# Kernel optimization log

Measured on AMD Instinct MI355X. Metric: run time of the kernel, lower is better.

The kernel has to match this reference:

```python
import jax, jax.numpy as jnp
import numpy as np

N_NODES = 100000
N_EDGES = 1600000
IN_FEATS = 128
HID = 128      # 2 * n_hidden
OUT = 64       # n_hidden


def setup_inputs() -> dict:
    key = jax.random.key(0)
    ks = jax.random.split(key, 10)
    features = jax.random.normal(ks[0], (N_NODES, IN_FEATS), dtype=jnp.float32)
    src = jax.random.randint(ks[1], (N_EDGES,), 0, N_NODES)
    dst = jax.random.randint(ks[2], (N_EDGES,), 0, N_NODES)
    s0 = 1.0 / np.sqrt(IN_FEATS)
    s1 = 1.0 / np.sqrt(HID)
    W_self0 = jax.random.uniform(ks[3], (IN_FEATS, HID), minval=-s0, maxval=s0, dtype=jnp.float32)
    W_neigh0 = jax.random.uniform(ks[4], (IN_FEATS, HID), minval=-s0, maxval=s0, dtype=jnp.float32)
    b0 = jnp.zeros((HID,), dtype=jnp.float32)
    W_self1 = jax.random.uniform(ks[5], (HID, OUT), minval=-s1, maxval=s1, dtype=jnp.float32)
    W_neigh1 = jax.random.uniform(ks[6], (HID, OUT), minval=-s1, maxval=s1, dtype=jnp.float32)
    b1 = jnp.zeros((OUT,), dtype=jnp.float32)
    return {"features": features, "src": src, "dst": dst,
            "W_self0": W_self0, "W_neigh0": W_neigh0, "b0": b0,
            "W_self1": W_self1, "W_neigh1": W_neigh1, "b1": b1}


def _mean_agg(x, src, dst, n_nodes):
    # gather neighbor feats along edges, sum per destination, divide by in-degree
    summed = jax.ops.segment_sum(x[src], dst, num_segments=n_nodes)  # [N, d]
    deg = jax.ops.segment_sum(jnp.ones((src.shape[0],), x.dtype), dst, num_segments=n_nodes)
    deg = jnp.maximum(deg, 1.0)[:, None]
    return summed / deg


def _sage_layer(x, src, dst, W_self, W_neigh, b, act):
    agg = _mean_agg(x, src, dst, x.shape[0])
    out = x @ W_self + agg @ W_neigh + b
    return jax.nn.relu(out) if act else out


def reference(features, src, dst, W_self0, W_neigh0, b0, W_self1, W_neigh1, b1):
    h = _sage_layer(features, src, dst, W_self0, W_neigh0, b0, act=True)
    h = _sage_layer(h, src, dst, W_self1, W_neigh1, b1, act=False)
    return h
```

## Files before the change

### kernel.cpp

```cpp
#include <hip/hip_runtime.h>

#define N_NODES 100000
#define N_EDGES 1600000
#define CAP 60
#define OVF_CAP 8192
#define GBLK 782
#define NBIN 1563
#define BINCAP2 1280
#define FBLK 12500
#define ZROW 100000

typedef unsigned int uint;
typedef unsigned short ushort;
typedef __attribute__((ext_vector_type(8))) short short8;
typedef __attribute__((ext_vector_type(4))) float f32x4;

__device__ __forceinline__ ushort f2bf(float f) {
  uint x = __float_as_uint(f);
  x += 0x7fffu + ((x >> 16) & 1u);
  return (ushort)(x >> 16);
}
__device__ __forceinline__ float bflo(uint u) {
  return __uint_as_float(u << 16);
}
__device__ __forceinline__ float bfhi(uint u) {
  return __uint_as_float(u & 0xffff0000u);
}
__device__ __forceinline__ f32x4 uplo(uint4 u) {
  return (f32x4){bflo(u.x), bfhi(u.x), bflo(u.y), bfhi(u.y)};
}
__device__ __forceinline__ f32x4 uphi(uint4 u) {
  return (f32x4){bflo(u.z), bfhi(u.z), bflo(u.w), bfhi(u.w)};
}

__global__ __launch_bounds__(256) void k_pb(
    const int* __restrict__ src, const int* __restrict__ dst,
    const float* __restrict__ feat, const float* __restrict__ Ws0,
    const float* __restrict__ Wn0, const float* __restrict__ Ws1,
    const float* __restrict__ Wn1, uint* __restrict__ gcursor,
    uint* __restrict__ binbuf, int* __restrict__ ovf_cnt,
    int* __restrict__ ovf, uint* __restrict__ fbfu, uint* __restrict__ hwu,
    ushort* __restrict__ wp0, ushort* __restrict__ wp1) {
  __shared__ uint hist[NBIN];
  int b = blockIdx.x;
  int tid = threadIdx.x;
  if (b < GBLK) {
    for (int i = tid; i < NBIN; i += 256) hist[i] = 0;
    __syncthreads();
    int e0 = b * 2048;
    uint val[8], bn[8], rk[8];
    int vld[8];
#pragma unroll
    for (int it = 0; it < 8; ++it) {
      int e = e0 + it * 256 + tid;
      vld[it] = (e < N_EDGES);
      if (vld[it]) {
        uint s = (uint)src[e];
        uint d = (uint)dst[e];
        bn[it] = d >> 6;
        rk[it] = atomicAdd(&hist[bn[it]], 1u);
        val[it] = s | ((d & 63u) << 17);
      }
    }
    __syncthreads();
    for (int i = tid; i < NBIN; i += 256) {
      uint h = hist[i];
      hist[i] = h ? atomicAdd(&gcursor[i * 16], h) : 0u;
    }
    __syncthreads();
#pragma unroll
    for (int it = 0; it < 8; ++it) {
      if (!vld[it]) continue;
      uint p = hist[bn[it]] + rk[it];
      if (p < BINCAP2) {
        binbuf[(size_t)bn[it] * BINCAP2 + p] = val[it];
      } else {
        int o = atomicAdd(ovf_cnt, 1);
        if (o < OVF_CAP) {
          ovf[2 * o] = (int)(val[it] & 0x1FFFFu);
          ovf[2 * o + 1] = (int)(bn[it] * 64 + (val[it] >> 17));
        }
      }
    }
    return;
  }
  if (b < GBLK + FBLK) {
    int i = (b - GBLK) * 256 + tid;
    float4 v = reinterpret_cast<const float4*>(feat)[i];
    uint2 o;
    o.x = (uint)f2bf(v.x) | ((uint)f2bf(v.y) << 16);
    o.y = (uint)f2bf(v.z) | ((uint)f2bf(v.w) << 16);
    reinterpret_cast<uint2*>(fbfu)[i] = o;
    return;
  }
  int wb = b - GBLK - FBLK;
  if (wb >= 192) {
    if (tid < 64) fbfu[ZROW * 64 + tid] = 0;
    else if (tid < 96) hwu[ZROW * 32 + (tid - 64)] = 0;
    return;
  }
  int idx = wb * 256 + tid;
  if (idx < 32768) {
    int k = idx >> 7, n = idx & 127;
    float v = (k < 128) ? Ws0[k * 128 + n] : Wn0[(k - 128) * 128 + n];
    int s = k >> 5, q = (k >> 3) & 3, j = k & 7;
    int t = n >> 4, c = n & 15;
    wp0[(((s * 8 + t) * 64) + (q * 16 + c)) * 8 + j] = f2bf(v);
  } else {
    int i2 = idx - 32768;
    int k = i2 >> 7, n = i2 & 127;
    float v = (n < 64) ? Wn1[k * 64 + n] : Ws1[k * 64 + (n - 64)];
    int s = k >> 5, q = (k >> 3) & 3, j = k & 7;
    int t = n >> 4, c = n & 15;
    wp1[(((s * 8 + t) * 64) + (q * 16 + c)) * 8 + j] = f2bf(v);
  }
}

__global__ __launch_bounds__(256) void k_agg0(
    const uint4* __restrict__ fbf4, const uint* __restrict__ binbuf,
    const uint* __restrict__ gcursor, int* __restrict__ ovf_cnt,
    int* __restrict__ ovf, uint4* __restrict__ agg4) {
  __shared__ __attribute__((aligned(16))) int lbkt[64 * CAP];
  __shared__ uint lcnt[64];
  int bb = blockIdx.x;
  int tid = threadIdx.x;
  if (tid < 64) lcnt[tid] = 0;
#pragma unroll
  for (int i = tid; i < 64 * CAP; i += 256) lbkt[i] = ZROW;
  __syncthreads();
  int ne = min((int)gcursor[bb * 16], BINCAP2);
  for (int i = tid; i < ne; i += 256) {
    uint v = binbuf[(size_t)bb * BINCAP2 + i];
    int ldl = (int)(v >> 17);
    uint pos = atomicAdd(&lcnt[ldl], 1u);
    if (pos < CAP) {
      lbkt[ldl * CAP + pos] = (int)(v & 0x1FFFFu);
    } else {
      int o = atomicAdd(ovf_cnt, 1);
      if (o < OVF_CAP) {
        ovf[2 * o] = (int)(v & 0x1FFFFu);
        ovf[2 * o + 1] = (bb * 64 + ldl) | (1 << 30);
      }
    }
  }
  __syncthreads();
  int g = tid >> 4, li = tid & 15;
  const int4* lb4 = reinterpret_cast<const int4*>(lbkt);
  int oc = min(*ovf_cnt, OVF_CAP);
#pragma unroll
  for (int p = 0; p < 4; ++p) {
    int nl = p * 16 + g;
    int n = bb * 64 + nl;
    int c = (int)lcnt[nl];
    int kb = min(c, CAP);
    f32x4 accA = (f32x4){0.f, 0.f, 0.f, 0.f};
    f32x4 accB = (f32x4){0.f, 0.f, 0.f, 0.f};
    for (int j = 0; j < kb; j += 12) {
      int4 ia = lb4[nl * 15 + (j >> 2)];
      int4 ib = lb4[nl * 15 + (j >> 2) + 1];
      int4 ic = lb4[nl * 15 + (j >> 2) + 2];
      uint4 u0 = fbf4[(size_t)ia.x * 16 + li];
      uint4 u1 = fbf4[(size_t)ia.y * 16 + li];
      uint4 u2 = fbf4[(size_t)ia.z * 16 + li];
      uint4 u3 = fbf4[(size_t)ia.w * 16 + li];
      uint4 u4 = fbf4[(size_t)ib.x * 16 + li];
      uint4 u5 = fbf4[(size_t)ib.y * 16 + li];
      uint4 u6 = fbf4[(size_t)ib.z * 16 + li];
      uint4 u7 = fbf4[(size_t)ib.w * 16 + li];
      uint4 u8 = fbf4[(size_t)ic.x * 16 + li];
      uint4 u9 = fbf4[(size_t)ic.y * 16 + li];
      uint4 ua = fbf4[(size_t)ic.z * 16 + li];
      uint4 ub = fbf4[(size_t)ic.w * 16 + li];
      accA += uplo(u0); accB += uphi(u0);
      accA += uplo(u1); accB += uphi(u1);
      accA += uplo(u2); accB += uphi(u2);
      accA += uplo(u3); accB += uphi(u3);
      accA += uplo(u4); accB += uphi(u4);
      accA += uplo(u5); accB += uphi(u5);
      accA += uplo(u6); accB += uphi(u6);
      accA += uplo(u7); accB += uphi(u7);
      accA += uplo(u8); accB += uphi(u8);
      accA += uplo(u9); accB += uphi(u9);
      accA += uplo(ua); accB += uphi(ua);
      accA += uplo(ub); accB += uphi(ub);
    }
    for (int i = 0; i < oc; ++i) {
      int df = ovf[2 * i + 1];
      if ((df & 0x1FFFF) == n) {
        uint4 u = fbf4[(size_t)ovf[2 * i] * 16 + li];
        accA += uplo(u);
        accB += uphi(u);
        c += ((df >> 30) & 1) ^ 1;
      }
    }
    float inv = 1.f / (float)max(c, 1);
    accA *= inv;
    accB *= inv;
    if (n < N_NODES) {
      uint4 o;
      o.x = (uint)f2bf(accA.x) | ((uint)f2bf(accA.y) << 16);
      o.y = (uint)f2bf(accA.z) | ((uint)f2bf(accA.w) << 16);
      o.z = (uint)f2bf(accB.x) | ((uint)f2bf(accB.y) << 16);
      o.w = (uint)f2bf(accB.z) | ((uint)f2bf(accB.w) << 16);
      agg4[(size_t)n * 16 + li] = o;
    }
  }
}

__global__ __launch_bounds__(256) void k_gemm(
    const ushort* __restrict__ fbf, const ushort* __restrict__ aggb,
    const short8* __restrict__ wp0f, const short8* __restrict__ wp1f,
    const float* __restrict__ b0, const float* __restrict__ b1,
    ushort* __restrict__ hw, float* __restrict__ out) {
  __shared__ ushort htile[128 * 128];
  int tid = threadIdx.x;
  int lane = tid & 63, w = tid >> 6;
  int quad = lane >> 4, lm = lane & 15;
  int rl0 = (w >> 1) * 64;
  int mw = blockIdx.x * 128 + rl0;
  int tgb = (w & 1) * 4;

  f32x4 acc[4][4];
#pragma unroll
  for (int rt = 0; rt < 4; ++rt)
#pragma unroll
    for (int ct = 0; ct < 4; ++ct) acc[rt][ct] = (f32x4){0.f, 0.f, 0.f, 0.f};
  short8 az = {0, 0, 0, 0, 0, 0, 0, 0};

#pragma unroll
  for (int s = 0; s < 8; ++s) {
    const ushort* bsrc = (s < 4) ? fbf : aggb;
    int koff = (s & 3) * 32 + quad * 8;
    short8 a[4];
#pragma unroll
    for (int rt = 0; rt < 4; ++rt) {
      int row = mw + rt * 16 + lm;
      a[rt] = (row < N_NODES)
                  ? *reinterpret_cast<const short8*>(bsrc + (size_t)row * 128 + koff)
                  : az;
    }
#pragma unroll
    for (int ct = 0; ct < 4; ++ct) {
      short8 b = wp0f[(s * 8 + tgb + ct) * 64 + lane];
#pragma unroll
      for (int rt = 0; rt < 4; ++rt)
        acc[rt][ct] =
            __builtin_amdgcn_mfma_f32_16x16x32_bf16(a[rt], b, acc[rt][ct], 0, 0, 0);
    }
  }

  {
    float bv[4];
#pragma unroll
    for (int ct = 0; ct < 4; ++ct) bv[ct] = b0[(tgb + ct) * 16 + lm];
#pragma unroll
    for (int rt = 0; rt < 4; ++rt)
#pragma unroll
      for (int ct = 0; ct < 4; ++ct)
#pragma unroll
        for (int i = 0; i < 4; ++i) {
          int r = rl0 + rt * 16 + quad * 4 + i;
          float v = (blockIdx.x * 128 + r < N_NODES)
                        ? fmaxf(acc[rt][ct][i] + bv[ct], 0.f)
                        : 0.f;
          int col = (tgb + ct) * 16 + lm;
          htile[r * 128 + (col ^ ((r & 15) * 8))] = f2bf(v);
        }
  }
  __syncthreads();

#pragma unroll
  for (int rt = 0; rt < 4; ++rt)
#pragma unroll
    for (int ct = 0; ct < 4; ++ct) acc[rt][ct] = (f32x4){0.f, 0.f, 0.f, 0.f};

#pragma unroll
  for (int s = 0; s < 4; ++s) {
    int koff = s * 32 + quad * 8;
    short8 a[4];
#pragma unroll
    for (int rt = 0; rt < 4; ++rt) {
      int r = rl0 + rt * 16 + lm;
      a[rt] = *reinterpret_cast<const short8*>(
          &htile[r * 128 + (koff ^ ((r & 15) * 8))]);
    }
#pragma unroll
    for (int ct = 0; ct < 4; ++ct) {
      short8 b = wp1f[(s * 8 + tgb + ct) * 64 + lane];
#pragma unroll
      for (int rt = 0; rt < 4; ++rt)
        acc[rt][ct] =
            __builtin_amdgcn_mfma_f32_16x16x32_bf16(a[rt], b, acc[rt][ct], 0, 0, 0);
    }
  }

  if ((w & 1) == 0) {
#pragma unroll
    for (int rt = 0; rt < 4; ++rt)
#pragma unroll
      for (int ct = 0; ct < 4; ++ct)
#pragma unroll
        for (int i = 0; i < 4; ++i) {
          int row = mw + rt * 16 + quad * 4 + i;
          if (row < N_NODES)
            hw[(size_t)row * 64 + ct * 16 + lm] = f2bf(acc[rt][ct][i]);
        }
  } else {
    float bv[4];
#pragma unroll
    for (int ct = 0; ct < 4; ++ct) bv[ct] = b1[ct * 16 + lm];
#pragma unroll
    for (int rt = 0; rt < 4; ++rt)
#pragma unroll
      for (int ct = 0; ct < 4; ++ct)
#pragma unroll
        for (int i = 0; i < 4; ++i) {
          int row = mw + rt * 16 + quad * 4 + i;
          if (row < N_NODES)
            out[(size_t)row * 64 + ct * 16 + lm] = acc[rt][ct][i] + bv[ct];
        }
  }
}

__global__ __launch_bounds__(256) void k_agg1(
    const uint4* __restrict__ hw4, const uint* __restrict__ binbuf,
    const uint* __restrict__ gcursor, int* __restrict__ ovf_cnt,
    int* __restrict__ ovf, float* __restrict__ out) {
  __shared__ __attribute__((aligned(16))) int lbkt[64 * CAP];
  __shared__ uint lcnt[64];
  int bb = blockIdx.x;
  int tid = threadIdx.x;
  if (tid < 64) lcnt[tid] = 0;
#pragma unroll
  for (int i = tid; i < 64 * CAP; i += 256) lbkt[i] = ZROW;
  __syncthreads();
  int ne = min((int)gcursor[bb * 16], BINCAP2);
  for (int i = tid; i < ne; i += 256) {
    uint v = binbuf[(size_t)bb * BINCAP2 + i];
    int ldl = (int)(v >> 17);
    uint pos = atomicAdd(&lcnt[ldl], 1u);
    if (pos < CAP) lbkt[ldl * CAP + pos] = (int)(v & 0x1FFFFu);
  }
  __syncthreads();
  int g = tid >> 3, li = tid & 7;
  const int4* lb4 = reinterpret_cast<const int4*>(lbkt);
  int oc = min(*ovf_cnt, OVF_CAP);
#pragma unroll
  for (int p = 0; p < 2; ++p) {
    int nl = p * 32 + g;
    int n = bb * 64 + nl;
    int c = (int)lcnt[nl];
    int kb = min(c, CAP);
    f32x4 accA = (f32x4){0.f, 0.f, 0.f, 0.f};
    f32x4 accB = (f32x4){0.f, 0.f, 0.f, 0.f};
    for (int j = 0; j < kb; j += 12) {
      int4 ia = lb4[nl * 15 + (j >> 2)];
      int4 ib = lb4[nl * 15 + (j >> 2) + 1];
      int4 ic = lb4[nl * 15 + (j >> 2) + 2];
      uint4 u0 = hw4[(size_t)ia.x * 8 + li];
      uint4 u1 = hw4[(size_t)ia.y * 8 + li];
      uint4 u2 = hw4[(size_t)ia.z * 8 + li];
      uint4 u3 = hw4[(size_t)ia.w * 8 + li];
      uint4 u4 = hw4[(size_t)ib.x * 8 + li];
      uint4 u5 = hw4[(size_t)ib.y * 8 + li];
      uint4 u6 = hw4[(size_t)ib.z * 8 + li];
      uint4 u7 = hw4[(size_t)ib.w * 8 + li];
      uint4 u8 = hw4[(size_t)ic.x * 8 + li];
      uint4 u9 = hw4[(size_t)ic.y * 8 + li];
      uint4 ua = hw4[(size_t)ic.z * 8 + li];
      uint4 ub = hw4[(size_t)ic.w * 8 + li];
      accA += uplo(u0); accB += uphi(u0);
      accA += uplo(u1); accB += uphi(u1);
      accA += uplo(u2); accB += uphi(u2);
      accA += uplo(u3); accB += uphi(u3);
      accA += uplo(u4); accB += uphi(u4);
      accA += uplo(u5); accB += uphi(u5);
      accA += uplo(u6); accB += uphi(u6);
      accA += uplo(u7); accB += uphi(u7);
      accA += uplo(u8); accB += uphi(u8);
      accA += uplo(u9); accB += uphi(u9);
      accA += uplo(ua); accB += uphi(ua);
      accA += uplo(ub); accB += uphi(ub);
    }
    for (int i = 0; i < oc; ++i) {
      int df = ovf[2 * i + 1];
      if ((df & 0x1FFFF) == n) {
        uint4 u = hw4[(size_t)ovf[2 * i] * 8 + li];
        accA += uplo(u);
        accB += uphi(u);
        c += ((df >> 30) & 1) ^ 1;
      }
    }
    if (n < N_NODES) {
      float inv = 1.f / (float)max(c, 1);
      float* op = out + (size_t)n * 64 + li * 8;
      float4 c0 = *reinterpret_cast<float4*>(op);
      float4 c1 = *reinterpret_cast<float4*>(op + 4);
      c0.x += accA.x * inv;
      c0.y += accA.y * inv;
      c0.z += accA.z * inv;
      c0.w += accA.w * inv;
      c1.x += accB.x * inv;
      c1.y += accB.y * inv;
      c1.z += accB.z * inv;
      c1.w += accB.w * inv;
      *reinterpret_cast<float4*>(op) = c0;
      *reinterpret_cast<float4*>(op + 4) = c1;
    }
  }
}

extern "C" void kernel_launch(void* const* d_in, const int* in_sizes, int n_in,
                              void* d_out, int out_size, void* d_ws,
                              size_t ws_size, hipStream_t stream) {
  const float* feat = (const float*)d_in[0];
  const int* src = (const int*)d_in[1];
  const int* dst = (const int*)d_in[2];
  const float* Ws0 = (const float*)d_in[3];
  const float* Wn0 = (const float*)d_in[4];
  const float* b0 = (const float*)d_in[5];
  const float* Ws1 = (const float*)d_in[6];
  const float* Wn1 = (const float*)d_in[7];
  const float* b1 = (const float*)d_in[8];
  char* ws = (char*)d_ws;

  ushort* hbuf = (ushort*)(ws);
  int* ovf_cnt = (int*)(ws + 25600000);
  uint* gcursor = (uint*)(ws + 25600064);
  int* ovf = (int*)(ws + 25700096);
  uint* binbuf = (uint*)(ws + 25765632);
  ushort* fbf = (ushort*)(ws + 33768192);
  ushort* hw = (ushort*)(ws + 59368448);
  ushort* wp0 = (ushort*)(ws + 72168576);
  ushort* wp1 = (ushort*)(ws + 72234112);
  float* out = (float*)d_out;

  hipMemsetAsync(ws + 25600000, 0, 100096, stream);
  k_pb<<<GBLK + FBLK + 193, 256, 0, stream>>>(
      src, dst, feat, Ws0, Wn0, Ws1, Wn1, gcursor, binbuf, ovf_cnt, ovf,
      (uint*)fbf, (uint*)hw, wp0, wp1);
  k_agg0<<<NBIN, 256, 0, stream>>>((const uint4*)fbf, binbuf, gcursor, ovf_cnt,
                                   ovf, (uint4*)hbuf);
  k_gemm<<<GBLK, 256, 0, stream>>>(fbf, hbuf, (const short8*)wp0,
                                   (const short8*)wp1, b0, b1, hw, out);
  k_agg1<<<NBIN, 256, 0, stream>>>((const uint4*)hw, binbuf, gcursor, ovf_cnt,
                                   ovf, out);
}
```

Before: 301.1 us.

## Split edge binning into coarse 1024-node buckets then a fine 64-node pass

Replaces the single-pass scatter of edges into 1563 fine bins with a two-level radix-style partition: the first pass scatters into 98 coarse buckets with fewer global atomics per block, and a new kernel splits each coarse bucket into 16 fine bins. This cuts global cursor atomic contention and the scattered, poorly coalesced writes across many bins. In exchange it adds an extra kernel launch and a full extra read/write of the edge list, and the coarse buffer reuses the hbuf region. The gcursor layout also drops its padding to 16-entry stride.

```diff
diff --git a/kernel.cpp b/kernel.cpp
--- a/kernel.cpp
+++ b/kernel.cpp
@@ -6,6 +6,8 @@
 #define OVF_CAP 8192
 #define GBLK 782
 #define NBIN 1563
+#define NCB 98
+#define CCAP 17408
 #define BINCAP2 1280
 #define FBLK 12500
 #define ZROW 100000
@@ -37,15 +39,15 @@
     const int* __restrict__ src, const int* __restrict__ dst,
     const float* __restrict__ feat, const float* __restrict__ Ws0,
     const float* __restrict__ Wn0, const float* __restrict__ Ws1,
-    const float* __restrict__ Wn1, uint* __restrict__ gcursor,
-    uint* __restrict__ binbuf, int* __restrict__ ovf_cnt,
+    const float* __restrict__ Wn1, uint* __restrict__ ccur,
+    uint* __restrict__ coarse, int* __restrict__ ovf_cnt,
     int* __restrict__ ovf, uint* __restrict__ fbfu, uint* __restrict__ hwu,
     ushort* __restrict__ wp0, ushort* __restrict__ wp1) {
-  __shared__ uint hist[NBIN];
+  __shared__ uint hist[NCB];
   int b = blockIdx.x;
   int tid = threadIdx.x;
   if (b < GBLK) {
-    for (int i = tid; i < NBIN; i += 256) hist[i] = 0;
+    if (tid < NCB) hist[tid] = 0;
     __syncthreads();
     int e0 = b * 2048;
     uint val[8], bn[8], rk[8];
@@ -57,28 +59,28 @@
       if (vld[it]) {
         uint s = (uint)src[e];
         uint d = (uint)dst[e];
-        bn[it] = d >> 6;
+        bn[it] = d >> 10;
         rk[it] = atomicAdd(&hist[bn[it]], 1u);
-        val[it] = s | ((d & 63u) << 17);
+        val[it] = s | ((d & 1023u) << 17);
       }
     }
     __syncthreads();
-    for (int i = tid; i < NBIN; i += 256) {
-      uint h = hist[i];
-      hist[i] = h ? atomicAdd(&gcursor[i * 16], h) : 0u;
+    if (tid < NCB) {
+      uint h = hist[tid];
+      hist[tid] = h ? atomicAdd(&ccur[tid], h) : 0u;
     }
     __syncthreads();
 #pragma unroll
     for (int it = 0; it < 8; ++it) {
       if (!vld[it]) continue;
       uint p = hist[bn[it]] + rk[it];
-      if (p < BINCAP2) {
-        binbuf[(size_t)bn[it] * BINCAP2 + p] = val[it];
+      if (p < CCAP) {
+        coarse[(size_t)bn[it] * CCAP + p] = val[it];
       } else {
         int o = atomicAdd(ovf_cnt, 1);
         if (o < OVF_CAP) {
           ovf[2 * o] = (int)(val[it] & 0x1FFFFu);
-          ovf[2 * o + 1] = (int)(bn[it] * 64 + (val[it] >> 17));
+          ovf[2 * o + 1] = (int)(bn[it] * 1024 + (val[it] >> 17));
         }
       }
     }
@@ -116,6 +118,56 @@
   }
 }
 
+__global__ __launch_bounds__(256) void k_fb(
+    const uint* __restrict__ coarse, const uint* __restrict__ ccur,
+    uint* __restrict__ gcursor, int* __restrict__ ovf_cnt,
+    int* __restrict__ ovf, uint* __restrict__ binbuf) {
+  __shared__ uint hist[16];
+  int blk = blockIdx.x;
+  int tid = threadIdx.x;
+  int cb = blk >> 4, q = blk & 15;
+  if (tid < 16) hist[tid] = 0;
+  __syncthreads();
+  int ne = min((int)ccur[cb], CCAP);
+  int lo = (q * ne) >> 4, hi = ((q + 1) * ne) >> 4;
+  uint val[5], rk[5];
+  int bnv[5], vld[5];
+#pragma unroll
+  for (int it = 0; it < 5; ++it) {
+    int i = lo + it * 256 + tid;
+    vld[it] = (i < hi);
+    if (vld[it]) {
+      uint v = coarse[(size_t)cb * CCAP + i];
+      uint d10 = v >> 17;
+      int f = (int)(d10 >> 6);
+      rk[it] = atomicAdd(&hist[f], 1u);
+      bnv[it] = f;
+      val[it] = (v & 0x1FFFFu) | ((d10 & 63u) << 17);
+    }
+  }
+  __syncthreads();
+  if (tid < 16) {
+    uint h = hist[tid];
+    hist[tid] = h ? atomicAdd(&gcursor[cb * 16 + tid], h) : 0u;
+  }
+  __syncthreads();
+#pragma unroll
+  for (int it = 0; it < 5; ++it) {
+    if (!vld[it]) continue;
+    uint p = hist[bnv[it]] + rk[it];
+    int fine = cb * 16 + bnv[it];
+    if (p < BINCAP2) {
+      binbuf[(size_t)fine * BINCAP2 + p] = val[it];
+    } else {
+      int o = atomicAdd(ovf_cnt, 1);
+      if (o < OVF_CAP) {
+        ovf[2 * o] = (int)(val[it] & 0x1FFFFu);
+        ovf[2 * o + 1] = fine * 64 + (int)(val[it] >> 17);
+      }
+    }
+  }
+}
+
 __global__ __launch_bounds__(256) void k_agg0(
     const uint4* __restrict__ fbf4, const uint* __restrict__ binbuf,
     const uint* __restrict__ gcursor, int* __restrict__ ovf_cnt,
@@ -128,7 +180,7 @@
 #pragma unroll
   for (int i = tid; i < 64 * CAP; i += 256) lbkt[i] = ZROW;
   __syncthreads();
-  int ne = min((int)gcursor[bb * 16], BINCAP2);
+  int ne = min((int)gcursor[bb], BINCAP2);
   for (int i = tid; i < ne; i += 256) {
     uint v = binbuf[(size_t)bb * BINCAP2 + i];
     int ldl = (int)(v >> 17);
@@ -334,7 +386,7 @@
 #pragma unroll
   for (int i = tid; i < 64 * CAP; i += 256) lbkt[i] = ZROW;
   __syncthreads();
-  int ne = min((int)gcursor[bb * 16], BINCAP2);
+  int ne = min((int)gcursor[bb], BINCAP2);
   for (int i = tid; i < ne; i += 256) {
     uint v = binbuf[(size_t)bb * BINCAP2 + i];
     int ldl = (int)(v >> 17);
@@ -425,20 +477,24 @@
   char* ws = (char*)d_ws;
 
   ushort* hbuf = (ushort*)(ws);
+  uint* coarse = (uint*)(ws);
   int* ovf_cnt = (int*)(ws + 25600000);
   uint* gcursor = (uint*)(ws + 25600064);
-  int* ovf = (int*)(ws + 25700096);
-  uint* binbuf = (uint*)(ws + 25765632);
-  ushort* fbf = (ushort*)(ws + 33768192);
-  ushort* hw = (ushort*)(ws + 59368448);
-  ushort* wp0 = (ushort*)(ws + 72168576);
-  ushort* wp1 = (ushort*)(ws + 72234112);
+  uint* ccur = (uint*)(ws + 25606336);
+  int* ovf = (int*)(ws + 25606784);
+  uint* binbuf = (uint*)(ws + 25672320);
+  ushort* fbf = (ushort*)(ws + 33674880);
+  ushort* hw = (ushort*)(ws + 59275136);
+  ushort* wp0 = (ushort*)(ws + 72075264);
+  ushort* wp1 = (ushort*)(ws + 72140800);
   float* out = (float*)d_out;
 
-  hipMemsetAsync(ws + 25600000, 0, 100096, stream);
+  hipMemsetAsync(ws + 25600000, 0, 6784, stream);
   k_pb<<<GBLK + FBLK + 193, 256, 0, stream>>>(
-      src, dst, feat, Ws0, Wn0, Ws1, Wn1, gcursor, binbuf, ovf_cnt, ovf,
+      src, dst, feat, Ws0, Wn0, Ws1, Wn1, ccur, coarse, ovf_cnt, ovf,
       (uint*)fbf, (uint*)hw, wp0, wp1);
+  k_fb<<<NCB * 16, 256, 0, stream>>>(coarse, ccur, gcursor, ovf_cnt, ovf,
+                                     binbuf);
   k_agg0<<<NBIN, 256, 0, stream>>>((const uint4*)fbf, binbuf, gcursor, ovf_cnt,
                                    ovf, (uint4*)hbuf);
   k_gemm<<<GBLK, 256, 0, stream>>>(fbf, hbuf, (const short8*)wp0,
```

Measured after the change: 272.2 us. 9.6% less time.
